# Optimization experiments

Hardware: AMD Instinct MI355X
Metric: run time of the kernel (lower is better)

## Reference

```python
import jax, jax.numpy as jnp
import numpy as np

# dims
B, L, D0, P, K = 4, 512, 640, 128, 16
C, H, NL = 32, 4, 3            # hidden channels, heads, layers
DH = C // H
RAD_IN = P + 2                 # pair feat + bppm + distance
HPT = 0.3                      # high_prob_threshold


def _build_edges(bppm, coords):
    """Backbone + kNN + high-prob edges per sample, deduped, flattened over batch."""
    src_all, dst_all = [], []
    for b in range(B):
        s_bb = np.arange(L - 1); d_bb = np.arange(1, L)
        srcs = [s_bb, d_bb]; dsts = [d_bb, s_bb]
        c = coords[b]
        d2 = ((c[:, None, :] - c[None, :, :]) ** 2).sum(-1)
        nn = np.argsort(d2, axis=1)[:, 1:K + 1]            # exclude self
        s_knn = np.repeat(np.arange(L), K); d_knn = nn.reshape(-1)
        srcs += [s_knn, d_knn]; dsts += [d_knn, s_knn]
        iu, ju = np.triu_indices(L, 2)                      # |i-j| > 1
        m = bppm[b][iu, ju] >= HPT
        hs, hd = iu[m], ju[m]
        srcs += [hs, hd]; dsts += [hd, hs]
        e = np.unique(np.stack([np.concatenate(srcs), np.concatenate(dsts)], 1), axis=0)
        src_all.append(e[:, 0] + b * L); dst_all.append(e[:, 1] + b * L)
    return np.concatenate(src_all).astype(np.int32), np.concatenate(dst_all).astype(np.int32)


def setup_inputs() -> dict:
    rng = np.random.default_rng(0)
    sequence_rep = rng.standard_normal((B, L, D0)).astype(np.float32)
    pair_rep = rng.standard_normal((B, L, L, P)).astype(np.float32)
    u = rng.random((B, L, L)).astype(np.float32)
    bppm = (0.5 * (u + u.transpose(0, 2, 1))) ** 8          # sparse-ish symmetric BPPM
    initial_coords = (10.0 * rng.standard_normal((B, L, 3))).astype(np.float32)
    edge_src, edge_dst = _build_edges(bppm, initial_coords)

    def w(*shape):
        fan = shape[-2] if len(shape) >= 2 else shape[-1]
        return (rng.standard_normal(shape) / np.sqrt(fan)).astype(np.float32)

    inp = dict(
        sequence_rep=jnp.asarray(sequence_rep), pair_rep=jnp.asarray(pair_rep),
        bppm=jnp.asarray(bppm.astype(np.float32)), initial_coords=jnp.asarray(initial_coords),
        edge_src=jnp.asarray(edge_src), edge_dst=jnp.asarray(edge_dst),
        Win0=jnp.asarray(w(D0, C)), Win1=jnp.asarray(w(1, C)),
        Wr1=jnp.asarray(w(NL, RAD_IN, 64)), br1=jnp.zeros((NL, 64), jnp.float32),
        Wr2=jnp.asarray(w(NL, 64, 4 * C)), br2=jnp.zeros((NL, 4 * C), jnp.float32),
        Wm00=jnp.asarray(w(NL, C, C)), Wm01=jnp.asarray(w(NL, C, C)),
        Wm10=jnp.asarray(w(NL, C, C)), Wm11=jnp.asarray(w(NL, C, C)),
        Wq=jnp.asarray(w(NL, C, C)), Wself0=jnp.asarray(w(NL, C, C)), Wself1=jnp.asarray(w(NL, C, C)),
        gamma0=jnp.ones((NL, C), jnp.float32), beta0=jnp.zeros((NL, C), jnp.float32),
        gamma1=jnp.ones((NL, C), jnp.float32), Wout=jnp.asarray(w(C, 1)),
    )
    return inp


def _forward(sequence_rep, pair_rep, bppm, initial_coords,
             Win0, Win1, Wr1, br1, Wr2, br2, Wm00, Wm01, Wm10, Wm11,
             Wq, Wself0, Wself1, gamma0, beta0, gamma1, Wout, edge_src, edge_dst):
    N = B * L
    x = initial_coords.reshape(N, 3)
    h0 = sequence_rep.reshape(N, D0) @ Win0                  # [N,C] degree-0
    h1 = x[:, None, :] * Win1[0][None, :, None]              # [N,C,3] degree-1
    src, dst = edge_src, edge_dst
    rel = x[dst] - x[src]
    r = jnp.sqrt(jnp.sum(rel * rel, -1) + 1e-12)             # [E]
    rhat = rel / (r[:, None] + 1e-8)                         # Y1 spherical harmonic dir
    b_idx, si, di = src // L, src % L, dst % L
    ef = jnp.concatenate([pair_rep[b_idx, si, di], bppm[b_idx, si, di][:, None], r[:, None]], -1)

    for l in range(NL):
        rad = jax.nn.relu(ef @ Wr1[l] + br1[l]) @ Wr2[l] + br2[l]   # [E,4C] radial weights
        w00, w01, w10, w11 = jnp.split(rad, 4, axis=-1)
        h0s, h1s = h0[src], h1[src]
        dot1 = jnp.einsum('ecd,ed->ec', h1s, rhat)                  # deg1 -> deg0 path
        m0 = w00 * (h0s @ Wm00[l]) + w01 * (dot1 @ Wm01[l])          # [E,C]
        m1 = (w11[:, :, None] * jnp.einsum('ecd,cf->efd', h1s, Wm11[l])
              + (w10 * (h0s @ Wm10[l]))[:, :, None] * rhat[:, None, :])  # [E,C,3]
        # multi-head attention over incoming edges
        q = (h0 @ Wq[l]).reshape(N, H, DH)
        k = m0.reshape(-1, H, DH)
        logit = jnp.sum(q[dst] * k, -1) / np.sqrt(DH)                # [E,H]
        mx = jax.ops.segment_max(logit, dst, num_segments=N)
        mx = jnp.where(jnp.isfinite(mx), mx, 0.0)
        a = jnp.exp(logit - mx[dst])
        den = jax.ops.segment_sum(a, dst, num_segments=N)
        alpha = a / (den[dst] + 1e-9)                                # [E,H]
        agg0 = jax.ops.segment_sum(alpha[:, :, None] * k, dst, num_segments=N).reshape(N, C)
        agg1 = jax.ops.segment_sum(alpha[:, :, None, None] * m1.reshape(-1, H, DH, 3),
                                   dst, num_segments=N).reshape(N, C, 3)
        h0 = h0 + agg0 @ Wself0[l]
        h1 = h1 + jnp.einsum('ncd,cf->nfd', agg1, Wself1[l])
        # norms: LayerNorm on deg-0, equivariant norm-gating on deg-1
        mu = h0.mean(-1, keepdims=True)
        h0 = (h0 - mu) / jnp.sqrt(h0.var(-1, keepdims=True) + 1e-5) * gamma0[l] + beta0[l]
        nrm = jnp.sqrt(jnp.sum(h1 * h1, -1) + 1e-12)                 # [N,C]
        nln = (nrm - nrm.mean(-1, keepdims=True)) / jnp.sqrt(nrm.var(-1, keepdims=True) + 1e-5) * gamma1[l]
        h1 = h1 * (nln / (nrm + 1e-8))[:, :, None]
    delta = jnp.einsum('ncd,co->nod', h1, Wout)[:, 0, :]             # fiber_out {'1':1}
    return (x + delta).reshape(B, L, 3)


def reference(sequence_rep, pair_rep, bppm, initial_coords, edge_src, edge_dst,
              Win0, Win1, Wr1, br1, Wr2, br2, Wm00, Wm01, Wm10, Wm11,
              Wq, Wself0, Wself1, gamma0, beta0, gamma1, Wout):
    return _forward(sequence_rep, pair_rep, bppm, initial_coords,
                    Win0, Win1, Wr1, br1, Wr2, br2, Wm00, Wm01, Wm10, Wm11,
                    Wq, Wself0, Wself1, gamma0, beta0, gamma1, Wout, edge_src, edge_dst)
```

## Files before the change

kernel.cpp:

```cpp
#include <hip/hip_runtime.h>
#include <hip/hip_bf16.h>
#include <math.h>

#define BB 4
#define LL 512
#define D0 640
#define PP 128
#define CC 32
#define NLAYER 3
#define NN (BB*LL)
#define RADIN 130

typedef __attribute__((ext_vector_type(8))) short bf16x8;
typedef __attribute__((ext_vector_type(4))) float f32x4;

__device__ __forceinline__ short f2b(float v) {
    __hip_bfloat16 h = __float2bfloat16(v);
    short s; __builtin_memcpy(&s, &h, 2); return s;
}


__global__ void k_zero_int(int* __restrict__ p, int n) {
    int i = blockIdx.x * blockDim.x + threadIdx.x;
    if (i < n) p[i] = 0;
}

__global__ __launch_bounds__(64) void k_init_h0(const float* __restrict__ seq,
                                                const float* __restrict__ Win0,
                                                float* __restrict__ h0) {
    const int n = blockIdx.x, lane = threadIdx.x;
    const int c = lane & 31, half = lane >> 5;
    const float* s = seq + (size_t)n * D0;
    float acc = 0.f;
    const int i0 = half * (D0 / 2), i1 = i0 + (D0 / 2);
    for (int i = i0; i < i1; ++i) acc = fmaf(s[i], Win0[i * CC + c], acc);
    acc += __shfl_xor(acc, 32);
    if (lane < 32) h0[n * CC + c] = acc;
}

__global__ void k_init_h1(const float* __restrict__ x, const float* __restrict__ Win1,
                          float* __restrict__ h1) {
    int idx = blockIdx.x * blockDim.x + threadIdx.x;
    if (idx >= NN * CC) return;
    int n = idx >> 5, c = idx & 31;
    float w = Win1[c];
    const float* xp = x + n * 3;
    float* hp = h1 + (size_t)n * 96 + c * 3;
    hp[0] = xp[0] * w; hp[1] = xp[1] * w; hp[2] = xp[2] * w;
}

__global__ void k_geom(const int* __restrict__ src, const int* __restrict__ dst,
                       const float* __restrict__ x, float* __restrict__ r_e,
                       float* __restrict__ rhat, int E) {
    int e = blockIdx.x * blockDim.x + threadIdx.x;
    if (e >= E) return;
    int s = src[e], d = dst[e];
    float dx = x[d * 3 + 0] - x[s * 3 + 0];
    float dy = x[d * 3 + 1] - x[s * 3 + 1];
    float dz = x[d * 3 + 2] - x[s * 3 + 2];
    float r = sqrtf(dx * dx + dy * dy + dz * dz + 1e-12f);
    float ir = 1.f / (r + 1e-8f);
    r_e[e] = r;
    rhat[e * 3 + 0] = dx * ir; rhat[e * 3 + 1] = dy * ir; rhat[e * 3 + 2] = dz * ir;
}

__global__ void k_count(const int* __restrict__ dst, int* __restrict__ deg, int E) {
    int e = blockIdx.x * blockDim.x + threadIdx.x;
    if (e < E) atomicAdd(&deg[dst[e]], 1);
}

__global__ __launch_bounds__(64) void k_scan(const int* __restrict__ deg,
                                             int* __restrict__ rowptr,
                                             int* __restrict__ cursor) {
    const int lane = threadIdx.x;
    const int base = lane * 32;
    int loc[32]; int s = 0;
    for (int i = 0; i < 32; ++i) { loc[i] = deg[base + i]; s += loc[i]; }
    int pre = s;
    for (int off = 1; off < 64; off <<= 1) {
        int t = __shfl_up(pre, off);
        if (lane >= off) pre += t;
    }
    pre -= s;
    int run = pre;
    for (int i = 0; i < 32; ++i) { rowptr[base + i] = run; cursor[base + i] = 0; run += loc[i]; }
    if (lane == 63) rowptr[NN] = run;
}

__global__ void k_scatter(const int* __restrict__ dst, const int* __restrict__ rowptr,
                          int* __restrict__ cursor, int* __restrict__ einc, int E) {
    int e = blockIdx.x * blockDim.x + threadIdx.x;
    if (e >= E) return;
    int d = dst[e];
    int pos = atomicAdd(&cursor[d], 1);
    einc[rowptr[d] + pos] = e;
}

__global__ __launch_bounds__(256) void k_build_ef(
    const int* __restrict__ src, const int* __restrict__ dst,
    const float* __restrict__ pair, const float* __restrict__ bppm,
    const float* __restrict__ r_e, short* __restrict__ efb, int E)
{
    int e = blockIdx.x * 4 + (threadIdx.x >> 6);
    int lane = threadIdx.x & 63;
    if (e >= E) return;
    int s = src[e], d = dst[e];
    int b = s / LL, si = s % LL, di = d % LL;
    size_t prow = ((size_t)b * LL + si) * LL + di;
    const float* pr = pair + prow * PP;
    short* out = efb + (size_t)e * 160;
    out[lane] = f2b(pr[lane]);
    out[64 + lane] = f2b(pr[64 + lane]);
    if (lane < 32) {
        int idx = 128 + lane;
        float v = 0.f;
        if (idx == 128) v = bppm[prow];
        else if (idx == 129) v = r_e[e];
        out[idx] = f2b(v);
    }
}

__global__ void k_pack(const float* __restrict__ Wr1, const float* __restrict__ Wr2,
                       short* __restrict__ W1p, short* __restrict__ W2p) {
    int t = blockIdx.x * blockDim.x + threadIdx.x;
    const int tot1 = NLAYER * 5 * 4 * 64 * 8;
    const int tot2 = NLAYER * 2 * 8 * 64 * 8;
    if (t < tot1) {
        int j = t & 7; int r = t >> 3;
        int ln = r & 63; r >>= 6;
        int cb = r & 3; r >>= 2;
        int kb = r % 5; int l = r / 5;
        int row = kb * 32 + (ln >> 4) * 8 + j;
        int col = cb * 16 + (ln & 15);
        float v = (row < RADIN) ? Wr1[((size_t)l * RADIN + row) * 64 + col] : 0.f;
        W1p[t] = f2b(v);
    } else if (t < tot1 + tot2) {
        int t2 = t - tot1;
        int j = t2 & 7; int r = t2 >> 3;
        int ln = r & 63; r >>= 6;
        int cb = r & 7; r >>= 3;
        int kb = r & 1; int l = r >> 1;
        int row = kb * 32 + (ln >> 4) * 8 + j;
        int col = cb * 16 + (ln & 15);
        W2p[t2] = f2b(Wr2[((size_t)l * 64 + row) * 128 + col]);
    }
}

__global__ __launch_bounds__(256) void k_nodepre(
    int l, const float* __restrict__ h0, const float* __restrict__ h1,
    const float* __restrict__ Wq, const float* __restrict__ Wm00,
    const float* __restrict__ Wm10, const float* __restrict__ Wm11,
    float* __restrict__ qbuf, float* __restrict__ P00,
    float* __restrict__ P10, float* __restrict__ P11)
{
    __shared__ float sh0[8][32], sh1[8][96];
    const int c = threadIdx.x & 31, hw = threadIdx.x >> 5;
    const int n = blockIdx.x * 8 + hw;
    sh0[hw][c] = h0[n * CC + c];
    const float* hp = h1 + (size_t)n * 96 + c * 3;
    sh1[hw][c * 3 + 0] = hp[0]; sh1[hw][c * 3 + 1] = hp[1]; sh1[hw][c * 3 + 2] = hp[2];
    const float* WqL  = Wq   + l * 1024;
    const float* W00L = Wm00 + l * 1024;
    const float* W10L = Wm10 + l * 1024;
    const float* W11L = Wm11 + l * 1024;
    float q = 0.f, p00 = 0.f, p10 = 0.f, px = 0.f, py = 0.f, pz = 0.f;
    for (int i = 0; i < 32; ++i) {
        float a = sh0[hw][i];
        q   = fmaf(a, WqL[i * 32 + c], q);
        p00 = fmaf(a, W00L[i * 32 + c], p00);
        p10 = fmaf(a, W10L[i * 32 + c], p10);
        float w = W11L[i * 32 + c];
        px = fmaf(sh1[hw][i * 3 + 0], w, px);
        py = fmaf(sh1[hw][i * 3 + 1], w, py);
        pz = fmaf(sh1[hw][i * 3 + 2], w, pz);
    }
    qbuf[n * 32 + c] = q; P00[n * 32 + c] = p00; P10[n * 32 + c] = p10;
    float* pp = P11 + (size_t)n * 96 + c * 3;
    pp[0] = px; pp[1] = py; pp[2] = pz;
}

__global__ __launch_bounds__(256) void k_radial(
    int l, int E,
    const short* __restrict__ efb,
    const short* __restrict__ W1p,
    const short* __restrict__ W2p,
    const float* __restrict__ br1,
    const float* __restrict__ br2,
    float* __restrict__ rad)
{
    __shared__ short s_hid[4][16][72];
    const int lane = threadIdx.x & 63, wv = threadIdx.x >> 6;
    const int r16 = lane & 15, q4 = lane >> 4;
    const int e0 = blockIdx.x * 64 + wv * 16;

    f32x4 acc0 = {0.f,0.f,0.f,0.f}, acc1 = {0.f,0.f,0.f,0.f};
    f32x4 acc2 = {0.f,0.f,0.f,0.f}, acc3 = {0.f,0.f,0.f,0.f};
    int row = e0 + r16; if (row >= E) row = E - 1;
    const short* arow = efb + (size_t)row * 160 + q4 * 8;
    const short* b1b = W1p + (size_t)l * (5 * 4 * 64 * 8) + lane * 8;
    for (int kb = 0; kb < 5; ++kb) {
        bf16x8 af = *(const bf16x8*)(arow + kb * 32);
        const short* bp = b1b + kb * (4 * 64 * 8);
        bf16x8 b0 = *(const bf16x8*)(bp);
        bf16x8 b1v = *(const bf16x8*)(bp + 64 * 8);
        bf16x8 b2v = *(const bf16x8*)(bp + 2 * 64 * 8);
        bf16x8 b3v = *(const bf16x8*)(bp + 3 * 64 * 8);
        acc0 = __builtin_amdgcn_mfma_f32_16x16x32_bf16(af, b0,  acc0, 0, 0, 0);
        acc1 = __builtin_amdgcn_mfma_f32_16x16x32_bf16(af, b1v, acc1, 0, 0, 0);
        acc2 = __builtin_amdgcn_mfma_f32_16x16x32_bf16(af, b2v, acc2, 0, 0, 0);
        acc3 = __builtin_amdgcn_mfma_f32_16x16x32_bf16(af, b3v, acc3, 0, 0, 0);
    }
    {
        f32x4 a[4] = {acc0, acc1, acc2, acc3};
        for (int cb = 0; cb < 4; ++cb) {
            int col = cb * 16 + r16;
            float b = br1[l * 64 + col];
            for (int i = 0; i < 4; ++i) {
                float v = fmaxf(a[cb][i] + b, 0.f);
                s_hid[wv][q4 * 4 + i][col] = f2b(v);
            }
        }
    }
    f32x4 o[8];
    for (int cb = 0; cb < 8; ++cb) { o[cb].x=0.f; o[cb].y=0.f; o[cb].z=0.f; o[cb].w=0.f; }
    const short* b2b = W2p + (size_t)l * (2 * 8 * 64 * 8) + lane * 8;
    for (int kb = 0; kb < 2; ++kb) {
        bf16x8 af = *(const bf16x8*)(&s_hid[wv][r16][kb * 32 + q4 * 8]);
        const short* bp = b2b + kb * (8 * 64 * 8);
        for (int cb = 0; cb < 8; ++cb) {
            bf16x8 bf = *(const bf16x8*)(bp + cb * (64 * 8));
            o[cb] = __builtin_amdgcn_mfma_f32_16x16x32_bf16(af, bf, o[cb], 0, 0, 0);
        }
    }
    for (int cb = 0; cb < 8; ++cb) {
        int col = cb * 16 + r16;
        float b = br2[l * 128 + col];
        for (int i = 0; i < 4; ++i) {
            int er = e0 + q4 * 4 + i;
            if (er < E) rad[(size_t)er * 128 + col] = o[cb][i] + b;
        }
    }
}

__global__ __launch_bounds__(256) void k_edge2(
    int l, int E, const int* __restrict__ src, const float* __restrict__ rhat,
    const float* __restrict__ rad, const float* __restrict__ h1,
    const float* __restrict__ Wm01, const float* __restrict__ P00,
    const float* __restrict__ P10, const float* __restrict__ P11,
    float* __restrict__ m0buf, float* __restrict__ m1buf)
{
    __shared__ float sW[1024];
    for (int i = threadIdx.x; i < 1024; i += 256) sW[i] = Wm01[l * 1024 + i];
    __syncthreads();
    const int e = blockIdx.x * 8 + (threadIdx.x >> 5);
    if (e >= E) return;
    const int c = threadIdx.x & 31;
    const int lane = threadIdx.x & 63;
    const int base = lane & 32;
    const int s = src[e];
    float r0 = rhat[e * 3 + 0], r1 = rhat[e * 3 + 1], r2 = rhat[e * 3 + 2];
    const float* hp = h1 + (size_t)s * 96 + c * 3;
    float dot = hp[0] * r0 + hp[1] * r1 + hp[2] * r2;
    float t1 = 0.f;
    for (int i = 0; i < 32; ++i) {
        float di = __shfl(dot, base + i);
        t1 = fmaf(di, sW[i * 32 + c], t1);
    }
    const float* rp = rad + (size_t)e * 128;
    float w00 = rp[c], w01 = rp[32 + c], w10 = rp[64 + c], w11 = rp[96 + c];
    m0buf[(size_t)e * 32 + c] = fmaf(w00, P00[s * 32 + c], w01 * t1);
    float u10 = w10 * P10[s * 32 + c];
    const float* pp = P11 + (size_t)s * 96 + c * 3;
    float* mp = m1buf + (size_t)e * 96 + c * 3;
    mp[0] = fmaf(w11, pp[0], u10 * r0);
    mp[1] = fmaf(w11, pp[1], u10 * r1);
    mp[2] = fmaf(w11, pp[2], u10 * r2);
}

__global__ __launch_bounds__(64) void k_node(
    int l, const int* __restrict__ rowptr, const int* __restrict__ einc,
    const float* __restrict__ m0buf, const float* __restrict__ m1buf,
    const float* __restrict__ qbuf,
    float* __restrict__ h0, float* __restrict__ h1,
    const float* __restrict__ Ws0, const float* __restrict__ Ws1,
    const float* __restrict__ gam0, const float* __restrict__ bet0,
    const float* __restrict__ gam1)
{
    const int n = blockIdx.x, lane = threadIdx.x;
    const int c = lane & 31, half = lane >> 5;
    __shared__ float s_h0[32], s_a0[32], s_a1[96];
    if (lane < 32) s_h0[lane] = h0[n * CC + lane];
    __syncthreads();

    float qc = qbuf[n * 32 + c];

    float m_run = -INFINITY, l_run = 0.f;
    float a0 = 0.f, a1x = 0.f, a1y = 0.f, a1z = 0.f;
    const int st = rowptr[n], en = rowptr[n + 1];
    for (int i = st; i < en; i += 2) {
        const int idx = i + half;
        const bool valid = idx < en;
        float kc = 0.f, mv0 = 0.f, mv1 = 0.f, mv2 = 0.f;
        if (valid) {
            const int e = einc[idx];
            kc = m0buf[(size_t)e * 32 + c];
            const float* mp = m1buf + (size_t)e * 96 + c * 3;
            mv0 = mp[0]; mv1 = mp[1]; mv2 = mp[2];
        }
        float p = qc * kc;
        p += __shfl_xor(p, 1); p += __shfl_xor(p, 2); p += __shfl_xor(p, 4);
        if (valid) {
            float logit = p * 0.35355339059327373f;
            float mn = fmaxf(m_run, logit);
            float sc = __expf(m_run - mn);
            float w  = __expf(logit - mn);
            l_run = fmaf(l_run, sc, w);
            a0  = fmaf(a0,  sc, w * kc);
            a1x = fmaf(a1x, sc, w * mv0);
            a1y = fmaf(a1y, sc, w * mv1);
            a1z = fmaf(a1z, sc, w * mv2);
            m_run = mn;
        }
    }
    float m_o  = __shfl_xor(m_run, 32), l_o = __shfl_xor(l_run, 32);
    float a0o  = __shfl_xor(a0, 32);
    float a1xo = __shfl_xor(a1x, 32), a1yo = __shfl_xor(a1y, 32), a1zo = __shfl_xor(a1z, 32);
    float mn = fmaxf(m_run, m_o);
    float sa = 0.f, sb = 0.f;
    if (mn > -INFINITY) { sa = __expf(m_run - mn); sb = __expf(m_o - mn); }
    float den = l_run * sa + l_o * sb;
    float inv = 1.0f / (den + 1e-9f);
    float g0c = (a0  * sa + a0o  * sb) * inv;
    float g1x = (a1x * sa + a1xo * sb) * inv;
    float g1y = (a1y * sa + a1yo * sb) * inv;
    float g1z = (a1z * sa + a1zo * sb) * inv;
    if (lane < 32) {
        s_a0[c] = g0c;
        s_a1[c * 3 + 0] = g1x; s_a1[c * 3 + 1] = g1y; s_a1[c * 3 + 2] = g1z;
    }
    __syncthreads();

    float x0 = s_h0[c];
    {
        const float* W = Ws0 + l * 1024;
        for (int i = 0; i < 32; ++i) x0 = fmaf(s_a0[i], W[i * 32 + c], x0);
    }
    float mu = x0;
    mu += __shfl_xor(mu, 1); mu += __shfl_xor(mu, 2); mu += __shfl_xor(mu, 4);
    mu += __shfl_xor(mu, 8); mu += __shfl_xor(mu, 16);
    mu *= (1.f / 32.f);
    float sq = x0 * x0;
    sq += __shfl_xor(sq, 1); sq += __shfl_xor(sq, 2); sq += __shfl_xor(sq, 4);
    sq += __shfl_xor(sq, 8); sq += __shfl_xor(sq, 16);
    float var = sq * (1.f / 32.f) - mu * mu;
    float h0n = (x0 - mu) * rsqrtf(var + 1e-5f) * gam0[l * 32 + c] + bet0[l * 32 + c];
    if (lane < 32) h0[n * CC + c] = h0n;

    const float* hp = h1 + (size_t)n * 96 + c * 3;
    float v0 = hp[0], v1 = hp[1], v2 = hp[2];
    {
        const float* W = Ws1 + l * 1024;
        for (int i = 0; i < 32; ++i) {
            float w = W[i * 32 + c];
            v0 = fmaf(s_a1[i * 3 + 0], w, v0);
            v1 = fmaf(s_a1[i * 3 + 1], w, v1);
            v2 = fmaf(s_a1[i * 3 + 2], w, v2);
        }
    }
    float nrm = sqrtf(v0 * v0 + v1 * v1 + v2 * v2 + 1e-12f);
    float mu2 = nrm;
    mu2 += __shfl_xor(mu2, 1); mu2 += __shfl_xor(mu2, 2); mu2 += __shfl_xor(mu2, 4);
    mu2 += __shfl_xor(mu2, 8); mu2 += __shfl_xor(mu2, 16);
    mu2 *= (1.f / 32.f);
    float sq2 = nrm * nrm;
    sq2 += __shfl_xor(sq2, 1); sq2 += __shfl_xor(sq2, 2); sq2 += __shfl_xor(sq2, 4);
    sq2 += __shfl_xor(sq2, 8); sq2 += __shfl_xor(sq2, 16);
    float var2 = sq2 * (1.f / 32.f) - mu2 * mu2;
    float nln = (nrm - mu2) * rsqrtf(var2 + 1e-5f) * gam1[l * 32 + c];
    float scl = nln / (nrm + 1e-8f);
    if (lane < 32) {
        float* hw = h1 + (size_t)n * 96 + c * 3;
        hw[0] = v0 * scl; hw[1] = v1 * scl; hw[2] = v2 * scl;
    }
}

__global__ void k_out(const float* __restrict__ x, const float* __restrict__ h1,
                      const float* __restrict__ Wout, float* __restrict__ out) {
    int idx = blockIdx.x * blockDim.x + threadIdx.x;
    if (idx >= NN * 3) return;
    int n = idx / 3, d = idx % 3;
    float acc = x[idx];
    const float* hp = h1 + (size_t)n * 96 + d;
    for (int cc = 0; cc < 32; ++cc) acc = fmaf(hp[cc * 3], Wout[cc], acc);
    out[idx] = acc;
}

extern "C" void kernel_launch(void* const* d_in, const int* in_sizes, int n_in,
                              void* d_out, int out_size, void* d_ws, size_t ws_size,
                              hipStream_t stream) {
    const float* seq  = (const float*)d_in[0];
    const float* pair = (const float*)d_in[1];
    const float* bppm = (const float*)d_in[2];
    const float* x    = (const float*)d_in[3];
    const int*   src  = (const int*)d_in[4];
    const int*   dst  = (const int*)d_in[5];
    const float* Win0 = (const float*)d_in[6];
    const float* Win1 = (const float*)d_in[7];
    const float* Wr1  = (const float*)d_in[8];
    const float* br1  = (const float*)d_in[9];
    const float* Wr2  = (const float*)d_in[10];
    const float* br2  = (const float*)d_in[11];
    const float* Wm00 = (const float*)d_in[12];
    const float* Wm01 = (const float*)d_in[13];
    const float* Wm10 = (const float*)d_in[14];
    const float* Wm11 = (const float*)d_in[15];
    const float* Wq   = (const float*)d_in[16];
    const float* Ws0  = (const float*)d_in[17];
    const float* Ws1  = (const float*)d_in[18];
    const float* gam0 = (const float*)d_in[19];
    const float* bet0 = (const float*)d_in[20];
    const float* gam1 = (const float*)d_in[21];
    const float* Wout = (const float*)d_in[22];
    const int E = in_sizes[4];

    char* w = (char*)d_ws;
    auto alloc = [&](size_t nbytes) {
        void* p = (void*)w;
        w += (nbytes + 255) & ~(size_t)255;
        return p;
    };
    float* h0    = (float*)alloc((size_t)NN * CC * 4);
    float* h1    = (float*)alloc((size_t)NN * CC * 3 * 4);
    float* r_e   = (float*)alloc((size_t)E * 4);
    float* rhat  = (float*)alloc((size_t)E * 3 * 4);
    float* m0buf = (float*)alloc((size_t)E * CC * 4);
    float* m1buf = (float*)alloc((size_t)E * CC * 3 * 4);
    int* deg     = (int*)alloc((size_t)NN * 4);
    int* rowptr  = (int*)alloc((size_t)(NN + 1) * 4);
    int* cursor  = (int*)alloc((size_t)NN * 4);
    int* einc    = (int*)alloc((size_t)E * 4);
    short* efb   = (short*)alloc((size_t)E * 160 * 2);
    short* W1p   = (short*)alloc((size_t)NLAYER * 5 * 4 * 64 * 8 * 2);
    short* W2p   = (short*)alloc((size_t)NLAYER * 2 * 8 * 64 * 8 * 2);
    float* rad   = (float*)alloc((size_t)E * 128 * 4);
    float* qbuf  = (float*)alloc((size_t)NN * 32 * 4);
    float* P00   = (float*)alloc((size_t)NN * 32 * 4);
    float* P10   = (float*)alloc((size_t)NN * 32 * 4);
    float* P11   = (float*)alloc((size_t)NN * 96 * 4);

    const int TB = 256;
    k_zero_int<<<(NN + TB - 1) / TB, TB, 0, stream>>>(deg, NN);
    k_init_h0<<<NN, 64, 0, stream>>>(seq, Win0, h0);
    k_init_h1<<<(NN * CC + TB - 1) / TB, TB, 0, stream>>>(x, Win1, h1);
    k_geom<<<(E + TB - 1) / TB, TB, 0, stream>>>(src, dst, x, r_e, rhat, E);
    k_count<<<(E + TB - 1) / TB, TB, 0, stream>>>(dst, deg, E);
    k_scan<<<1, 64, 0, stream>>>(deg, rowptr, cursor);
    k_scatter<<<(E + TB - 1) / TB, TB, 0, stream>>>(dst, rowptr, cursor, einc, E);
    k_build_ef<<<(E + 3) / 4, 256, 0, stream>>>(src, dst, pair, bppm, r_e, efb, E);
    {
        int tot = NLAYER * 5 * 4 * 64 * 8 + NLAYER * 2 * 8 * 64 * 8;
        k_pack<<<(tot + TB - 1) / TB, TB, 0, stream>>>(Wr1, Wr2, W1p, W2p);
    }

    for (int l = 0; l < NLAYER; ++l) {
        k_nodepre<<<NN / 8, 256, 0, stream>>>(l, h0, h1, Wq, Wm00, Wm10, Wm11,
                                              qbuf, P00, P10, P11);
        k_radial<<<(E + 63) / 64, 256, 0, stream>>>(l, E, efb, W1p, W2p, br1, br2, rad);
        k_edge2<<<(E + 7) / 8, 256, 0, stream>>>(l, E, src, rhat, rad, h1, Wm01,
                                                 P00, P10, P11, m0buf, m1buf);
        k_node<<<NN, 64, 0, stream>>>(l, rowptr, einc, m0buf, m1buf, qbuf, h0, h1,
                                      Ws0, Ws1, gam0, bet0, gam1);
    }
    k_out<<<(NN * 3 + TB - 1) / TB, TB, 0, stream>>>(x, h1, Wout, (float*)d_out);
}
```

Measured before the change: 899.7 us.

## Build CSR by binary search, fuse node pre/out stages, batch radial MLP across layers

Drops the atomic count/scan/scatter CSR build. Instead, row pointers come from a binary search over the sorted src array, and a reverse-edge slot is found per edge, so k_edge2 writes messages directly in destination-grouped order. Next-layer node projections and the final output projection are fused into k_node, and the radial MLP for all three layers is computed in one launch that keeps edge features in registers. The radial GEMMs now use a split-bf16 hi/lo three-pass scheme for better accuracy, which triples the MFMA work and doubles the edge-feature storage. The CSR shortcut depends on edges being sorted by (src,dst) and symmetric, both of which the edge builder guarantees.

```diff
diff --git a/kernel.cpp b/kernel.cpp
--- a/kernel.cpp
+++ b/kernel.cpp
@@ -18,12 +18,16 @@
     __hip_bfloat16 h = __float2bfloat16(v);
     short s; __builtin_memcpy(&s, &h, 2); return s;
 }
-
-
-__global__ void k_zero_int(int* __restrict__ p, int n) {
-    int i = blockIdx.x * blockDim.x + threadIdx.x;
-    if (i < n) p[i] = 0;
-}
+__device__ __forceinline__ float b2f(short s) {
+    unsigned int u = ((unsigned int)(unsigned short)s) << 16;
+    float f; __builtin_memcpy(&f, &u, 4); return f;
+}
+__device__ __forceinline__ void fsplit(float v, short* hi, short* lo) {
+    short h = f2b(v);
+    *hi = h;
+    *lo = f2b(v - b2f(h));
+}
+
 
 __global__ __launch_bounds__(64) void k_init_h0(const float* __restrict__ seq,
                                                 const float* __restrict__ Win0,
@@ -64,42 +68,28 @@
     rhat[e * 3 + 0] = dx * ir; rhat[e * 3 + 1] = dy * ir; rhat[e * 3 + 2] = dz * ir;
 }
 
-__global__ void k_count(const int* __restrict__ dst, int* __restrict__ deg, int E) {
-    int e = blockIdx.x * blockDim.x + threadIdx.x;
-    if (e < E) atomicAdd(&deg[dst[e]], 1);
-}
-
-__global__ __launch_bounds__(64) void k_scan(const int* __restrict__ deg,
-                                             int* __restrict__ rowptr,
-                                             int* __restrict__ cursor) {
-    const int lane = threadIdx.x;
-    const int base = lane * 32;
-    int loc[32]; int s = 0;
-    for (int i = 0; i < 32; ++i) { loc[i] = deg[base + i]; s += loc[i]; }
-    int pre = s;
-    for (int off = 1; off < 64; off <<= 1) {
-        int t = __shfl_up(pre, off);
-        if (lane >= off) pre += t;
-    }
-    pre -= s;
-    int run = pre;
-    for (int i = 0; i < 32; ++i) { rowptr[base + i] = run; cursor[base + i] = 0; run += loc[i]; }
-    if (lane == 63) rowptr[NN] = run;
-}
-
-__global__ void k_scatter(const int* __restrict__ dst, const int* __restrict__ rowptr,
-                          int* __restrict__ cursor, int* __restrict__ einc, int E) {
+__global__ void k_rowptr(const int* __restrict__ src, int* __restrict__ rowptr, int E) {
+    int n = blockIdx.x * blockDim.x + threadIdx.x;
+    if (n > NN) return;
+    int lo = 0, hi = E;
+    while (lo < hi) { int mid = (lo + hi) >> 1; if (src[mid] < n) lo = mid + 1; else hi = mid; }
+    rowptr[n] = lo;
+}
+
+__global__ void k_rev(const int* __restrict__ src, const int* __restrict__ dst,
+                      const int* __restrict__ rowptr, int* __restrict__ rev, int E) {
     int e = blockIdx.x * blockDim.x + threadIdx.x;
     if (e >= E) return;
-    int d = dst[e];
-    int pos = atomicAdd(&cursor[d], 1);
-    einc[rowptr[d] + pos] = e;
+    int s = src[e], d = dst[e];
+    int lo = rowptr[d], hi = rowptr[d + 1];
+    while (lo < hi) { int mid = (lo + hi) >> 1; if (dst[mid] < s) lo = mid + 1; else hi = mid; }
+    rev[e] = lo;
 }
 
 __global__ __launch_bounds__(256) void k_build_ef(
     const int* __restrict__ src, const int* __restrict__ dst,
     const float* __restrict__ pair, const float* __restrict__ bppm,
-    const float* __restrict__ r_e, short* __restrict__ efb, int E)
+    const float* __restrict__ r_e, short* __restrict__ efh, short* __restrict__ efl, int E)
 {
     int e = blockIdx.x * 4 + (threadIdx.x >> 6);
     int lane = threadIdx.x & 63;
@@ -108,23 +98,27 @@
     int b = s / LL, si = s % LL, di = d % LL;
     size_t prow = ((size_t)b * LL + si) * LL + di;
     const float* pr = pair + prow * PP;
-    short* out = efb + (size_t)e * 160;
-    out[lane] = f2b(pr[lane]);
-    out[64 + lane] = f2b(pr[64 + lane]);
+    short* oh = efh + (size_t)e * 160;
+    short* ol = efl + (size_t)e * 160;
+    short hi, lo;
+    fsplit(pr[lane], &hi, &lo); oh[lane] = hi; ol[lane] = lo;
+    fsplit(pr[64 + lane], &hi, &lo); oh[64 + lane] = hi; ol[64 + lane] = lo;
     if (lane < 32) {
         int idx = 128 + lane;
         float v = 0.f;
         if (idx == 128) v = bppm[prow];
         else if (idx == 129) v = r_e[e];
-        out[idx] = f2b(v);
+        fsplit(v, &hi, &lo); oh[idx] = hi; ol[idx] = lo;
     }
 }
 
 __global__ void k_pack(const float* __restrict__ Wr1, const float* __restrict__ Wr2,
-                       short* __restrict__ W1p, short* __restrict__ W2p) {
+                       short* __restrict__ W1h, short* __restrict__ W1l,
+                       short* __restrict__ W2h, short* __restrict__ W2l) {
     int t = blockIdx.x * blockDim.x + threadIdx.x;
     const int tot1 = NLAYER * 5 * 4 * 64 * 8;
     const int tot2 = NLAYER * 2 * 8 * 64 * 8;
+    short hi, lo;
     if (t < tot1) {
         int j = t & 7; int r = t >> 3;
         int ln = r & 63; r >>= 6;
@@ -133,7 +127,7 @@
         int row = kb * 32 + (ln >> 4) * 8 + j;
         int col = cb * 16 + (ln & 15);
         float v = (row < RADIN) ? Wr1[((size_t)l * RADIN + row) * 64 + col] : 0.f;
-        W1p[t] = f2b(v);
+        fsplit(v, &hi, &lo); W1h[t] = hi; W1l[t] = lo;
     } else if (t < tot1 + tot2) {
         int t2 = t - tot1;
         int j = t2 & 7; int r = t2 >> 3;
@@ -142,7 +136,8 @@
         int kb = r & 1; int l = r >> 1;
         int row = kb * 32 + (ln >> 4) * 8 + j;
         int col = cb * 16 + (ln & 15);
-        W2p[t2] = f2b(Wr2[((size_t)l * 64 + row) * 128 + col]);
+        float v = Wr2[((size_t)l * 64 + row) * 128 + col];
+        fsplit(v, &hi, &lo); W2h[t2] = hi; W2l[t2] = lo;
     }
 }
 
@@ -179,74 +174,89 @@
     pp[0] = px; pp[1] = py; pp[2] = pz;
 }
 
-__global__ __launch_bounds__(256) void k_radial(
-    int l, int E,
-    const short* __restrict__ efb,
-    const short* __restrict__ W1p,
-    const short* __restrict__ W2p,
-    const float* __restrict__ br1,
-    const float* __restrict__ br2,
-    float* __restrict__ rad)
+__global__ __launch_bounds__(256) void k_radial3(
+    int E,
+    const short* __restrict__ efh, const short* __restrict__ efl,
+    const short* __restrict__ W1h, const short* __restrict__ W1l,
+    const short* __restrict__ W2h, const short* __restrict__ W2l,
+    const float* __restrict__ br1, const float* __restrict__ br2,
+    float* __restrict__ rad3)
 {
-    __shared__ short s_hid[4][16][72];
+    __shared__ short s_hh[4][16][72], s_hl[4][16][72];
     const int lane = threadIdx.x & 63, wv = threadIdx.x >> 6;
     const int r16 = lane & 15, q4 = lane >> 4;
     const int e0 = blockIdx.x * 64 + wv * 16;
-
-    f32x4 acc0 = {0.f,0.f,0.f,0.f}, acc1 = {0.f,0.f,0.f,0.f};
-    f32x4 acc2 = {0.f,0.f,0.f,0.f}, acc3 = {0.f,0.f,0.f,0.f};
     int row = e0 + r16; if (row >= E) row = E - 1;
-    const short* arow = efb + (size_t)row * 160 + q4 * 8;
-    const short* b1b = W1p + (size_t)l * (5 * 4 * 64 * 8) + lane * 8;
-    for (int kb = 0; kb < 5; ++kb) {
-        bf16x8 af = *(const bf16x8*)(arow + kb * 32);
-        const short* bp = b1b + kb * (4 * 64 * 8);
-        bf16x8 b0 = *(const bf16x8*)(bp);
-        bf16x8 b1v = *(const bf16x8*)(bp + 64 * 8);
-        bf16x8 b2v = *(const bf16x8*)(bp + 2 * 64 * 8);
-        bf16x8 b3v = *(const bf16x8*)(bp + 3 * 64 * 8);
-        acc0 = __builtin_amdgcn_mfma_f32_16x16x32_bf16(af, b0,  acc0, 0, 0, 0);
-        acc1 = __builtin_amdgcn_mfma_f32_16x16x32_bf16(af, b1v, acc1, 0, 0, 0);
-        acc2 = __builtin_amdgcn_mfma_f32_16x16x32_bf16(af, b2v, acc2, 0, 0, 0);
-        acc3 = __builtin_amdgcn_mfma_f32_16x16x32_bf16(af, b3v, acc3, 0, 0, 0);
-    }
+
+    bf16x8 ah[5], al[5];
     {
-        f32x4 a[4] = {acc0, acc1, acc2, acc3};
+        const short* arh = efh + (size_t)row * 160 + q4 * 8;
+        const short* arl = efl + (size_t)row * 160 + q4 * 8;
+        for (int kb = 0; kb < 5; ++kb) {
+            ah[kb] = *(const bf16x8*)(arh + kb * 32);
+            al[kb] = *(const bf16x8*)(arl + kb * 32);
+        }
+    }
+
+    for (int l = 0; l < NLAYER; ++l) {
+        f32x4 acc[4];
+        for (int cb = 0; cb < 4; ++cb) { acc[cb][0]=0.f; acc[cb][1]=0.f; acc[cb][2]=0.f; acc[cb][3]=0.f; }
+        const short* b1h = W1h + (size_t)l * 10240 + lane * 8;
+        const short* b1l = W1l + (size_t)l * 10240 + lane * 8;
+        for (int kb = 0; kb < 5; ++kb) {
+            for (int cb = 0; cb < 4; ++cb) {
+                bf16x8 bh = *(const bf16x8*)(b1h + (kb * 4 + cb) * 512);
+                bf16x8 bl = *(const bf16x8*)(b1l + (kb * 4 + cb) * 512);
+                acc[cb] = __builtin_amdgcn_mfma_f32_16x16x32_bf16(ah[kb], bh, acc[cb], 0, 0, 0);
+                acc[cb] = __builtin_amdgcn_mfma_f32_16x16x32_bf16(al[kb], bh, acc[cb], 0, 0, 0);
+                acc[cb] = __builtin_amdgcn_mfma_f32_16x16x32_bf16(ah[kb], bl, acc[cb], 0, 0, 0);
+            }
+        }
+        __syncthreads();
         for (int cb = 0; cb < 4; ++cb) {
             int col = cb * 16 + r16;
             float b = br1[l * 64 + col];
             for (int i = 0; i < 4; ++i) {
-                float v = fmaxf(a[cb][i] + b, 0.f);
-                s_hid[wv][q4 * 4 + i][col] = f2b(v);
+                float h = fmaxf(acc[cb][i] + b, 0.f);
+                short hh = f2b(h);
+                s_hh[wv][q4 * 4 + i][col] = hh;
+                s_hl[wv][q4 * 4 + i][col] = f2b(h - b2f(hh));
             }
         }
-    }
-    f32x4 o[8];
-    for (int cb = 0; cb < 8; ++cb) { o[cb].x=0.f; o[cb].y=0.f; o[cb].z=0.f; o[cb].w=0.f; }
-    const short* b2b = W2p + (size_t)l * (2 * 8 * 64 * 8) + lane * 8;
-    for (int kb = 0; kb < 2; ++kb) {
-        bf16x8 af = *(const bf16x8*)(&s_hid[wv][r16][kb * 32 + q4 * 8]);
-        const short* bp = b2b + kb * (8 * 64 * 8);
+        __syncthreads();
+        f32x4 o[8];
+        for (int cb = 0; cb < 8; ++cb) { o[cb][0]=0.f; o[cb][1]=0.f; o[cb][2]=0.f; o[cb][3]=0.f; }
+        const short* b2h = W2h + (size_t)l * 8192 + lane * 8;
+        const short* b2l = W2l + (size_t)l * 8192 + lane * 8;
+        for (int kb = 0; kb < 2; ++kb) {
+            bf16x8 a2h = *(const bf16x8*)(&s_hh[wv][r16][kb * 32 + q4 * 8]);
+            bf16x8 a2l = *(const bf16x8*)(&s_hl[wv][r16][kb * 32 + q4 * 8]);
+            for (int cb = 0; cb < 8; ++cb) {
+                bf16x8 bh = *(const bf16x8*)(b2h + (kb * 8 + cb) * 512);
+                bf16x8 bl = *(const bf16x8*)(b2l + (kb * 8 + cb) * 512);
+                o[cb] = __builtin_amdgcn_mfma_f32_16x16x32_bf16(a2h, bh, o[cb], 0, 0, 0);
+                o[cb] = __builtin_amdgcn_mfma_f32_16x16x32_bf16(a2l, bh, o[cb], 0, 0, 0);
+                o[cb] = __builtin_amdgcn_mfma_f32_16x16x32_bf16(a2h, bl, o[cb], 0, 0, 0);
+            }
+        }
+        float* radl = rad3 + (size_t)l * E * 128;
         for (int cb = 0; cb < 8; ++cb) {
-            bf16x8 bf = *(const bf16x8*)(bp + cb * (64 * 8));
-            o[cb] = __builtin_amdgcn_mfma_f32_16x16x32_bf16(af, bf, o[cb], 0, 0, 0);
-        }
-    }
-    for (int cb = 0; cb < 8; ++cb) {
-        int col = cb * 16 + r16;
-        float b = br2[l * 128 + col];
-        for (int i = 0; i < 4; ++i) {
-            int er = e0 + q4 * 4 + i;
-            if (er < E) rad[(size_t)er * 128 + col] = o[cb][i] + b;
+            int col = cb * 16 + r16;
+            float b = br2[l * 128 + col];
+            for (int i = 0; i < 4; ++i) {
+                int er = e0 + q4 * 4 + i;
+                if (er < E) radl[(size_t)er * 128 + col] = o[cb][i] + b;
+            }
         }
     }
 }
 
 __global__ __launch_bounds__(256) void k_edge2(
-    int l, int E, const int* __restrict__ src, const float* __restrict__ rhat,
-    const float* __restrict__ rad, const float* __restrict__ h1,
-    const float* __restrict__ Wm01, const float* __restrict__ P00,
-    const float* __restrict__ P10, const float* __restrict__ P11,
+    int l, int E, const int* __restrict__ src, const int* __restrict__ rev,
+    const float* __restrict__ rhat, const float* __restrict__ rad3,
+    const float* __restrict__ h1, const float* __restrict__ Wm01,
+    const float* __restrict__ P00, const float* __restrict__ P10,
+    const float* __restrict__ P11,
     float* __restrict__ m0buf, float* __restrict__ m1buf)
 {
     __shared__ float sW[1024];
@@ -258,6 +268,7 @@
     const int lane = threadIdx.x & 63;
     const int base = lane & 32;
     const int s = src[e];
+    const int slot = rev[e];
     float r0 = rhat[e * 3 + 0], r1 = rhat[e * 3 + 1], r2 = rhat[e * 3 + 2];
     const float* hp = h1 + (size_t)s * 96 + c * 3;
     float dot = hp[0] * r0 + hp[1] * r1 + hp[2] * r2;
@@ -266,25 +277,31 @@
         float di = __shfl(dot, base + i);
         t1 = fmaf(di, sW[i * 32 + c], t1);
     }
-    const float* rp = rad + (size_t)e * 128;
+    const float* rp = rad3 + ((size_t)l * E + e) * 128;
     float w00 = rp[c], w01 = rp[32 + c], w10 = rp[64 + c], w11 = rp[96 + c];
-    m0buf[(size_t)e * 32 + c] = fmaf(w00, P00[s * 32 + c], w01 * t1);
+    m0buf[(size_t)slot * 32 + c] = fmaf(w00, P00[s * 32 + c], w01 * t1);
     float u10 = w10 * P10[s * 32 + c];
     const float* pp = P11 + (size_t)s * 96 + c * 3;
-    float* mp = m1buf + (size_t)e * 96 + c * 3;
+    float* mp = m1buf + (size_t)slot * 96 + c * 3;
     mp[0] = fmaf(w11, pp[0], u10 * r0);
     mp[1] = fmaf(w11, pp[1], u10 * r1);
     mp[2] = fmaf(w11, pp[2], u10 * r2);
 }
 
 __global__ __launch_bounds__(64) void k_node(
-    int l, const int* __restrict__ rowptr, const int* __restrict__ einc,
+    int l, int lnext, int last, const int* __restrict__ rowptr,
     const float* __restrict__ m0buf, const float* __restrict__ m1buf,
     const float* __restrict__ qbuf,
     float* __restrict__ h0, float* __restrict__ h1,
     const float* __restrict__ Ws0, const float* __restrict__ Ws1,
     const float* __restrict__ gam0, const float* __restrict__ bet0,
-    const float* __restrict__ gam1)
+    const float* __restrict__ gam1,
+    const float* __restrict__ Wq, const float* __restrict__ Wm00,
+    const float* __restrict__ Wm10, const float* __restrict__ Wm11,
+    float* __restrict__ qout, float* __restrict__ P00,
+    float* __restrict__ P10, float* __restrict__ P11,
+    const float* __restrict__ x, const float* __restrict__ Wout,
+    float* __restrict__ out)
 {
     const int n = blockIdx.x, lane = threadIdx.x;
     const int c = lane & 31, half = lane >> 5;
@@ -302,9 +319,8 @@
         const bool valid = idx < en;
         float kc = 0.f, mv0 = 0.f, mv1 = 0.f, mv2 = 0.f;
         if (valid) {
-            const int e = einc[idx];
-            kc = m0buf[(size_t)e * 32 + c];
-            const float* mp = m1buf + (size_t)e * 96 + c * 3;
+            kc = m0buf[(size_t)idx * 32 + c];
+            const float* mp = m1buf + (size_t)idx * 96 + c * 3;
             mv0 = mp[0]; mv1 = mp[1]; mv2 = mp[2];
         }
         float p = qc * kc;
@@ -378,21 +394,50 @@
     float var2 = sq2 * (1.f / 32.f) - mu2 * mu2;
     float nln = (nrm - mu2) * rsqrtf(var2 + 1e-5f) * gam1[l * 32 + c];
     float scl = nln / (nrm + 1e-8f);
+    __syncthreads();
     if (lane < 32) {
         float* hw = h1 + (size_t)n * 96 + c * 3;
-        hw[0] = v0 * scl; hw[1] = v1 * scl; hw[2] = v2 * scl;
-    }
-}
-
-__global__ void k_out(const float* __restrict__ x, const float* __restrict__ h1,
-                      const float* __restrict__ Wout, float* __restrict__ out) {
-    int idx = blockIdx.x * blockDim.x + threadIdx.x;
-    if (idx >= NN * 3) return;
-    int n = idx / 3, d = idx % 3;
-    float acc = x[idx];
-    const float* hp = h1 + (size_t)n * 96 + d;
-    for (int cc = 0; cc < 32; ++cc) acc = fmaf(hp[cc * 3], Wout[cc], acc);
-    out[idx] = acc;
+        float n0 = v0 * scl, n1 = v1 * scl, n2 = v2 * scl;
+        hw[0] = n0; hw[1] = n1; hw[2] = n2;
+        s_h0[c] = h0n;
+        s_a1[c * 3 + 0] = n0; s_a1[c * 3 + 1] = n1; s_a1[c * 3 + 2] = n2;
+    }
+    __syncthreads();
+
+    if (!last) {
+        if (lane < 32) {
+            const float* WqL  = Wq   + lnext * 1024;
+            const float* W00L = Wm00 + lnext * 1024;
+            const float* W10L = Wm10 + lnext * 1024;
+            float q = 0.f, p00 = 0.f, p10 = 0.f;
+            for (int i = 0; i < 32; ++i) {
+                float a = s_h0[i];
+                q   = fmaf(a, WqL[i * 32 + c], q);
+                p00 = fmaf(a, W00L[i * 32 + c], p00);
+                p10 = fmaf(a, W10L[i * 32 + c], p10);
+            }
+            qout[n * 32 + c] = q; P00[n * 32 + c] = p00; P10[n * 32 + c] = p10;
+        } else {
+            const int f = lane - 32;
+            const float* W11L = Wm11 + lnext * 1024;
+            float px = 0.f, py = 0.f, pz = 0.f;
+            for (int i = 0; i < 32; ++i) {
+                float w = W11L[i * 32 + f];
+                px = fmaf(s_a1[i * 3 + 0], w, px);
+                py = fmaf(s_a1[i * 3 + 1], w, py);
+                pz = fmaf(s_a1[i * 3 + 2], w, pz);
+            }
+            float* pp = P11 + (size_t)n * 96 + f * 3;
+            pp[0] = px; pp[1] = py; pp[2] = pz;
+        }
+    } else {
+        if (lane < 3) {
+            const int d = lane;
+            float acc = x[n * 3 + d];
+            for (int i = 0; i < 32; ++i) acc = fmaf(s_a1[i * 3 + d], Wout[i], acc);
+            out[n * 3 + d] = acc;
+        }
+    }
 }
 
 extern "C" void kernel_launch(void* const* d_in, const int* in_sizes, int n_in,
@@ -435,41 +480,43 @@
     float* rhat  = (float*)alloc((size_t)E * 3 * 4);
     float* m0buf = (float*)alloc((size_t)E * CC * 4);
     float* m1buf = (float*)alloc((size_t)E * CC * 3 * 4);
-    int* deg     = (int*)alloc((size_t)NN * 4);
     int* rowptr  = (int*)alloc((size_t)(NN + 1) * 4);
-    int* cursor  = (int*)alloc((size_t)NN * 4);
-    int* einc    = (int*)alloc((size_t)E * 4);
-    short* efb   = (short*)alloc((size_t)E * 160 * 2);
-    short* W1p   = (short*)alloc((size_t)NLAYER * 5 * 4 * 64 * 8 * 2);
-    short* W2p   = (short*)alloc((size_t)NLAYER * 2 * 8 * 64 * 8 * 2);
-    float* rad   = (float*)alloc((size_t)E * 128 * 4);
+    int* rev     = (int*)alloc((size_t)E * 4);
+    short* efh   = (short*)alloc((size_t)E * 160 * 2);
+    short* efl   = (short*)alloc((size_t)E * 160 * 2);
+    short* W1h   = (short*)alloc((size_t)NLAYER * 10240 * 2);
+    short* W1l   = (short*)alloc((size_t)NLAYER * 10240 * 2);
+    short* W2h   = (short*)alloc((size_t)NLAYER * 8192 * 2);
+    short* W2l   = (short*)alloc((size_t)NLAYER * 8192 * 2);
+    float* rad3  = (float*)alloc((size_t)NLAYER * E * 128 * 4);
     float* qbuf  = (float*)alloc((size_t)NN * 32 * 4);
     float* P00   = (float*)alloc((size_t)NN * 32 * 4);
     float* P10   = (float*)alloc((size_t)NN * 32 * 4);
     float* P11   = (float*)alloc((size_t)NN * 96 * 4);
 
     const int TB = 256;
-    k_zero_int<<<(NN + TB - 1) / TB, TB, 0, stream>>>(deg, NN);
     k_init_h0<<<NN, 64, 0, stream>>>(seq, Win0, h0);
     k_init_h1<<<(NN * CC + TB - 1) / TB, TB, 0, stream>>>(x, Win1, h1);
     k_geom<<<(E + TB - 1) / TB, TB, 0, stream>>>(src, dst, x, r_e, rhat, E);
-    k_count<<<(E + TB - 1) / TB, TB, 0, stream>>>(dst, deg, E);
-    k_scan<<<1, 64, 0, stream>>>(deg, rowptr, cursor);
-    k_scatter<<<(E + TB - 1) / TB, TB, 0, stream>>>(dst, rowptr, cursor, einc, E);
-    k_build_ef<<<(E + 3) / 4, 256, 0, stream>>>(src, dst, pair, bppm, r_e, efb, E);
+    k_rowptr<<<(NN + 1 + TB - 1) / TB, TB, 0, stream>>>(src, rowptr, E);
+    k_rev<<<(E + TB - 1) / TB, TB, 0, stream>>>(src, dst, rowptr, rev, E);
+    k_build_ef<<<(E + 3) / 4, 256, 0, stream>>>(src, dst, pair, bppm, r_e, efh, efl, E);
     {
-        int tot = NLAYER * 5 * 4 * 64 * 8 + NLAYER * 2 * 8 * 64 * 8;
-        k_pack<<<(tot + TB - 1) / TB, TB, 0, stream>>>(Wr1, Wr2, W1p, W2p);
-    }
+        int tot = NLAYER * 10240 + NLAYER * 8192;
+        k_pack<<<(tot + TB - 1) / TB, TB, 0, stream>>>(Wr1, Wr2, W1h, W1l, W2h, W2l);
+    }
+    k_nodepre<<<NN / 8, 256, 0, stream>>>(0, h0, h1, Wq, Wm00, Wm10, Wm11,
+                                          qbuf, P00, P10, P11);
+    k_radial3<<<(E + 63) / 64, 256, 0, stream>>>(E, efh, efl, W1h, W1l, W2h, W2l,
+                                                 br1, br2, rad3);
 
     for (int l = 0; l < NLAYER; ++l) {
-        k_nodepre<<<NN / 8, 256, 0, stream>>>(l, h0, h1, Wq, Wm00, Wm10, Wm11,
-                                              qbuf, P00, P10, P11);
-        k_radial<<<(E + 63) / 64, 256, 0, stream>>>(l, E, efb, W1p, W2p, br1, br2, rad);
-        k_edge2<<<(E + 7) / 8, 256, 0, stream>>>(l, E, src, rhat, rad, h1, Wm01,
+        k_edge2<<<(E + 7) / 8, 256, 0, stream>>>(l, E, src, rev, rhat, rad3, h1, Wm01,
                                                  P00, P10, P11, m0buf, m1buf);
-        k_node<<<NN, 64, 0, stream>>>(l, rowptr, einc, m0buf, m1buf, qbuf, h0, h1,
-                                      Ws0, Ws1, gam0, bet0, gam1);
-    }
-    k_out<<<(NN * 3 + TB - 1) / TB, TB, 0, stream>>>(x, h1, Wout, (float*)d_out);
-}
+        k_node<<<NN, 64, 0, stream>>>(l, l + 1, (l == NLAYER - 1) ? 1 : 0, rowptr,
+                                      m0buf, m1buf, qbuf, h0, h1,
+                                      Ws0, Ws1, gam0, bet0, gam1,
+                                      Wq, Wm00, Wm10, Wm11, qbuf, P00, P10, P11,
+                                      x, Wout, (float*)d_out);
+    }
+}
```

Result: no change. 908.6 us (+1.0%).
